# Optimization experiments

Hardware: AMD Instinct MI355X
Metric: run time of the kernel (lower is better)

## Reference

```python
import jax, jax.numpy as jnp
import numpy as np

V, C, L, D, H = 50257, 512, 6, 768, 12
HD = D // H
B, T = 4, 512
EPS = 1e-5


def setup_inputs() -> dict:
    key = jax.random.key(0)
    ks = jax.random.split(key, 24)
    s = 0.02
    inp = {
        'x': jax.random.randint(ks[0], (B, T), 0, V),
        'target': jax.random.randint(ks[1], (B, T), 0, V),
        'tok_emb': jax.random.normal(ks[2], (V, D), jnp.float32) * s,
        'pos_emb': jax.random.normal(ks[3], (C, D), jnp.float32) * s,
        'in_proj_w': jax.random.normal(ks[4], (L, D, D), jnp.float32) * s,
        'in_proj_b': jnp.zeros((L, D), jnp.float32),
        'wk': jax.random.normal(ks[5], (L, H, D, HD), jnp.float32) * s,
        'bk': jnp.zeros((L, H, HD), jnp.float32),
        'wq': jax.random.normal(ks[6], (L, H, D, HD), jnp.float32) * s,
        'bq': jnp.zeros((L, H, HD), jnp.float32),
        'wv': jax.random.normal(ks[7], (L, H, D, HD), jnp.float32) * s,
        'bv': jnp.zeros((L, H, HD), jnp.float32),
        'out_proj_w': jax.random.normal(ks[8], (L, D, D), jnp.float32) * s,
        'out_proj_b': jnp.zeros((L, D), jnp.float32),
        'ff_w1': jax.random.normal(ks[9], (L, D, 4 * D), jnp.float32) * s,
        'ff_b1': jnp.zeros((L, 4 * D), jnp.float32),
        'ff_w2': jax.random.normal(ks[10], (L, 4 * D, D), jnp.float32) * s,
        'ff_b2': jnp.zeros((L, D), jnp.float32),
        'lna_g': jnp.ones((L, D), jnp.float32),
        'lna_b': jnp.zeros((L, D), jnp.float32),
        'lnf_g': jnp.ones((L, D), jnp.float32),
        'lnf_b': jnp.zeros((L, D), jnp.float32),
        'out_w': jax.random.normal(ks[11], (D, V), jnp.float32) * s,
        'out_b': jnp.zeros((V,), jnp.float32),
    }
    return inp


def _ln(x, g, b):
    m = jnp.mean(x, axis=-1, keepdims=True)
    v = jnp.var(x, axis=-1, keepdims=True)
    return (x - m) * jax.lax.rsqrt(v + EPS) * g + b


def _gpt(x_ids, tok_emb, pos_emb, in_proj_w, in_proj_b, wk, bk, wq, bq, wv, bv,
         out_proj_w, out_proj_b, ff_w1, ff_b1, ff_w2, ff_b2,
         lna_g, lna_b, lnf_g, lnf_b, out_w, out_b):
    t = x_ids.shape[1]
    x = tok_emb[x_ids] + pos_emb[:t]  # [B,T,D]
    causal = jnp.tril(jnp.ones((t, t), bool))  # mask[t,s]
    for l in range(L):
        h = _ln(x, lna_g[l], lna_b[l])
        h = h @ in_proj_w[l] + in_proj_b[l]
        k = jnp.einsum('btd,hde->bhte', h, wk[l]) + bk[l][None, :, None, :]
        q = jnp.einsum('btd,hde->bhte', h, wq[l]) + bq[l][None, :, None, :]
        v = jnp.einsum('btd,hde->bhte', h, wv[l]) + bv[l][None, :, None, :]
        # Faithful quirk: scores = k @ q^T, NO 1/sqrt(d) scaling
        wei = jnp.einsum('bhte,bhse->bhts', k, q)
        wei = jnp.where(causal, wei, -jnp.inf)
        wei = jax.nn.softmax(wei, axis=-1)
        attn = jnp.einsum('bhts,bhse->bhte', wei, v)  # [B,H,T,HD]
        attn = attn.transpose(0, 2, 1, 3).reshape(x.shape[0], t, D)
        x = attn @ out_proj_w[l] + out_proj_b[l] + x
        h = _ln(x, lnf_g[l], lnf_b[l])
        h = jax.nn.relu(h @ ff_w1[l] + ff_b1[l]) @ ff_w2[l] + ff_b2[l]
        x = h + x
    logits = x @ out_w + out_b  # [B,T,V]
    return logits


def reference(x, target, tok_emb, pos_emb, in_proj_w, in_proj_b, wk, bk, wq, bq,
              wv, bv, out_proj_w, out_proj_b, ff_w1, ff_b1, ff_w2, ff_b2,
              lna_g, lna_b, lnf_g, lnf_b, out_w, out_b):
    logits = _gpt(x, tok_emb, pos_emb, in_proj_w, in_proj_b, wk, bk, wq, bq,
                  wv, bv, out_proj_w, out_proj_b, ff_w1, ff_b1, ff_w2, ff_b2,
                  lna_g, lna_b, lnf_g, lnf_b, out_w, out_b)
    logp = jax.nn.log_softmax(logits.reshape(-1, V), axis=-1)
    nll = -jnp.take_along_axis(logp, target.reshape(-1, 1), axis=-1)
    loss = jnp.mean(nll)
    return logits, loss
```

## Files before the change

### kernel.cpp

```cpp
#include <hip/hip_runtime.h>
#include <cstdint>
#include <cstddef>

static constexpr int kD   = 768;
static constexpr int kHD  = 64;
static constexpr int kNH  = 12;
static constexpr int kT   = 512;
static constexpr int kB   = 4;
static constexpr int kRows = kB * kT;
static constexpr int kV   = 50257;
static constexpr int kL   = 6;
static constexpr int kFF  = 3072;
static constexpr float kEps = 1e-5f;

typedef short bf16x8 __attribute__((ext_vector_type(8)));
typedef float f32x4  __attribute__((ext_vector_type(4)));
typedef unsigned short u16;
typedef unsigned short u16x4 __attribute__((ext_vector_type(4)));
typedef unsigned short u16x8 __attribute__((ext_vector_type(8)));

__device__ __forceinline__ void split1(float a, u16& h, u16& l)
{
    unsigned u = __float_as_uint(a);
    h = (u16)(u >> 16);
    float fh = __uint_as_float(u & 0xFFFF0000u);
    float r = a - fh;
    unsigned v = __float_as_uint(r);
    l = (u16)((v + 0x7FFFu + ((v >> 16) & 1u)) >> 16);
}

__global__ __launch_bounds__(256) void embed_kernel(
    const int* __restrict__ ids, const float* __restrict__ tok,
    const float* __restrict__ pos, float* __restrict__ x)
{
    int i = blockIdx.x * 256 + threadIdx.x;
    if (i >= kRows * kD) return;
    int row = i / kD, d = i - row * kD;
    x[i] = tok[(size_t)ids[row] * kD + d] + pos[(row % kT) * kD + d];
}

__global__ __launch_bounds__(256) void ln_kernel(
    const float* __restrict__ x, const float* __restrict__ g,
    const float* __restrict__ b, float* __restrict__ o)
{
    const int row = blockIdx.x;
    const float* xr = x + (size_t)row * kD;
    float s = 0.f, ss = 0.f;
    for (int d = threadIdx.x; d < kD; d += 256) {
        float v = xr[d];
        s += v; ss += v * v;
    }
    #pragma unroll
    for (int off = 32; off; off >>= 1) {
        s  += __shfl_xor(s, off);
        ss += __shfl_xor(ss, off);
    }
    __shared__ float sh_s[4], sh_ss[4];
    const int wid = threadIdx.x >> 6, lane = threadIdx.x & 63;
    if (lane == 0) { sh_s[wid] = s; sh_ss[wid] = ss; }
    __syncthreads();
    s  = sh_s[0] + sh_s[1] + sh_s[2] + sh_s[3];
    ss = sh_ss[0] + sh_ss[1] + sh_ss[2] + sh_ss[3];
    const float mean = s * (1.0f / kD);
    const float var  = ss * (1.0f / kD) - mean * mean;
    const float rstd = rsqrtf(var + kEps);
    float* orow = o + (size_t)row * kD;
    for (int d = threadIdx.x; d < kD; d += 256)
        orow[d] = (xr[d] - mean) * rstd * g[d] + b[d];
}

__global__ __launch_bounds__(256) void split_kernel(
    const float* __restrict__ in, u16* __restrict__ hi, u16* __restrict__ lo)
{
    const int i = blockIdx.x * 256 + threadIdx.x;
    float4 v = ((const float4*)in)[i];
    u16x4 hv, lv;
    u16 a, c;
    split1(v.x, a, c); hv[0] = a; lv[0] = c;
    split1(v.y, a, c); hv[1] = a; lv[1] = c;
    split1(v.z, a, c); hv[2] = a; lv[2] = c;
    split1(v.w, a, c); hv[3] = a; lv[3] = c;
    ((u16x4*)hi)[i] = hv;
    ((u16x4*)lo)[i] = lv;
}

__global__ __launch_bounds__(256) void repack_qkv_kernel(
    const float* __restrict__ wk, const float* __restrict__ wq,
    const float* __restrict__ wv, const float* __restrict__ bk,
    const float* __restrict__ bq, const float* __restrict__ bv,
    float* __restrict__ Wp, float* __restrict__ Bp)
{
    int i = blockIdx.x * 256 + threadIdx.x;
    if (i < 3 * kD) {
        int which = i / kD, c = i - which * kD;
        const float* bsrc = (which == 0) ? bk : (which == 1) ? bq : bv;
        Bp[i] = bsrc[c];
    }
    if (i >= kD * 3 * kD) return;
    int col = i % (3 * kD), d = i / (3 * kD);
    int which = col / kD, hc = col - which * kD;
    const float* src = (which == 0) ? wk : (which == 1) ? wq : wv;
    Wp[i] = src[(size_t)(hc >> 6) * (kD * kHD) + (size_t)d * kHD + (hc & 63)];
}

template<int BM>
__global__ __launch_bounds__(256) void gemm3_kernel(
    const u16* __restrict__ Ahi, const u16* __restrict__ Alo,
    const float* __restrict__ W, const float* __restrict__ bias,
    const float* __restrict__ resid, float* __restrict__ out,
    int N, int K, int relu)
{
    constexpr int LDT = 40;
    __shared__ u16 Ah[BM][LDT], Al[BM][LDT];
    __shared__ u16 Bh[128][LDT], Bl[128][LDT];
    const int tid = threadIdx.x;
    const int m0 = blockIdx.y * BM;
    const int n0 = blockIdx.x * 128;
    const int wid = tid >> 6, lane = tid & 63;
    const int wr = wid >> 1, wc = wid & 1;
    const int fr = lane & 15, fg = lane >> 4;
    constexpr int MF = BM / 32;

    f32x4 acc[MF][4];
    #pragma unroll
    for (int i = 0; i < MF; ++i)
        #pragma unroll
        for (int j = 0; j < 4; ++j) acc[i][j] = (f32x4){0.f, 0.f, 0.f, 0.f};

    const int bc  = tid >> 1;
    const int bk0 = (tid & 1) << 4;
    const bool bvalid = (n0 + bc) < N;

    for (int k0 = 0; k0 < K; k0 += 32) {
        for (int i = tid; i < BM * 4; i += 256) {
            const int r = i >> 2, q = (i & 3) << 3;
            const size_t off = (size_t)(m0 + r) * K + k0 + q;
            *(u16x8*)&Ah[r][q] = *(const u16x8*)(Ahi + off);
            *(u16x8*)&Al[r][q] = *(const u16x8*)(Alo + off);
        }
        {
            const float* wp = W + (size_t)(k0 + bk0) * N + (n0 + bc);
            float v[16];
            #pragma unroll
            for (int j = 0; j < 16; ++j)
                v[j] = bvalid ? wp[(size_t)j * N] : 0.f;
            #pragma unroll
            for (int j4 = 0; j4 < 4; ++j4) {
                u16x4 hh, ll;
                #pragma unroll
                for (int j = 0; j < 4; ++j) {
                    u16 h1, l1; split1(v[(j4 << 2) + j], h1, l1);
                    hh[j] = h1; ll[j] = l1;
                }
                *(u16x4*)&Bh[bc][bk0 + (j4 << 2)] = hh;
                *(u16x4*)&Bl[bc][bk0 + (j4 << 2)] = ll;
            }
        }
        __syncthreads();

        bf16x8 ah[MF], al[MF], bh[4], bl[4];
        #pragma unroll
        for (int f = 0; f < MF; ++f) {
            const int row = wr * (BM / 2) + (f << 4) + fr;
            ah[f] = *(const bf16x8*)&Ah[row][fg << 3];
            al[f] = *(const bf16x8*)&Al[row][fg << 3];
        }
        #pragma unroll
        for (int f = 0; f < 4; ++f) {
            const int col = (wc << 6) + (f << 4) + fr;
            bh[f] = *(const bf16x8*)&Bh[col][fg << 3];
            bl[f] = *(const bf16x8*)&Bl[col][fg << 3];
        }
        #pragma unroll
        for (int i = 0; i < MF; ++i)
            #pragma unroll
            for (int j = 0; j < 4; ++j) {
                acc[i][j] = __builtin_amdgcn_mfma_f32_16x16x32_bf16(ah[i], bh[j], acc[i][j], 0, 0, 0);
                acc[i][j] = __builtin_amdgcn_mfma_f32_16x16x32_bf16(ah[i], bl[j], acc[i][j], 0, 0, 0);
                acc[i][j] = __builtin_amdgcn_mfma_f32_16x16x32_bf16(al[i], bh[j], acc[i][j], 0, 0, 0);
            }
        __syncthreads();
    }

    #pragma unroll
    for (int i = 0; i < MF; ++i) {
        const int mb = m0 + wr * (BM / 2) + (i << 4) + (fg << 2);
        #pragma unroll
        for (int j = 0; j < 4; ++j) {
            const int n = n0 + (wc << 6) + (j << 4) + fr;
            if (n < N) {
                const float bvv = bias ? bias[n] : 0.f;
                #pragma unroll
                for (int r = 0; r < 4; ++r) {
                    const size_t oo = (size_t)(mb + r) * N + n;
                    float vv = acc[i][j][r] + bvv;
                    if (resid) vv += resid[oo];
                    if (relu)  vv = fmaxf(vv, 0.f);
                    out[oo] = vv;
                }
            }
        }
    }
}

__global__ __launch_bounds__(256) void attn2_kernel(
    const float* __restrict__ qkv, float* __restrict__ out)
{
    __shared__ float KbT[64][64];
    __shared__ float QbT[64][64];
    __shared__ float Vb[64][64];
    __shared__ float Pt[64][64];
    const int tb = gridDim.x - 1 - blockIdx.x;
    const int hh = blockIdx.y, b = blockIdx.z;
    const int t0 = tb << 6;
    const int tid = threadIdx.x;
    const int ty = tid >> 4, tx = tid & 15;
    const int sr = tid >> 2;
    const int se0 = (tid & 3) << 4;
    const size_t rb = (size_t)b * kT;

    {
        const float* ks = qkv + (rb + t0 + sr) * (3 * kD) + hh * kHD + se0;
        #pragma unroll
        for (int j = 0; j < 16; j += 4) {
            float4 v = *(const float4*)(ks + j);
            KbT[se0 + j + 0][sr] = v.x;
            KbT[se0 + j + 1][sr] = v.y;
            KbT[se0 + j + 2][sr] = v.z;
            KbT[se0 + j + 3][sr] = v.w;
        }
    }

    float m[4], l[4], O[4][4];
    #pragma unroll
    for (int i = 0; i < 4; ++i) {
        m[i] = -INFINITY; l[i] = 0.f;
        #pragma unroll
        for (int j = 0; j < 4; ++j) O[i][j] = 0.f;
    }

    for (int s0 = 0; s0 <= t0; s0 += 64) {
        __syncthreads();
        {
            const float* qs = qkv + (rb + s0 + sr) * (3 * kD) + kD + hh * kHD + se0;
            #pragma unroll
            for (int j = 0; j < 16; j += 4) {
                float4 v = *(const float4*)(qs + j);
                QbT[se0 + j + 0][sr] = v.x;
                QbT[se0 + j + 1][sr] = v.y;
                QbT[se0 + j + 2][sr] = v.z;
                QbT[se0 + j + 3][sr] = v.w;
            }
            const float* vs = qkv + (rb + s0 + sr) * (3 * kD) + 2 * kD + hh * kHD + se0;
            #pragma unroll
            for (int jq = 0; jq < 4; ++jq) {
                const int c4 = (se0 >> 2) + jq;
                *(float4*)&Vb[sr][(c4 ^ (sr & 15)) << 2] = *(const float4*)(vs + (jq << 2));
            }
        }
        __syncthreads();

        float S[4][4];
        #pragma unroll
        for (int i = 0; i < 4; ++i)
            #pragma unroll
            for (int j = 0; j < 4; ++j) S[i][j] = 0.f;

        #pragma unroll 8
        for (int e = 0; e < 64; ++e) {
            float4 ka = *(const float4*)&KbT[e][ty << 2];
            float4 qa = *(const float4*)&QbT[e][tx << 2];
            float a[4] = {ka.x, ka.y, ka.z, ka.w};
            float q[4] = {qa.x, qa.y, qa.z, qa.w};
            #pragma unroll
            for (int i = 0; i < 4; ++i)
                #pragma unroll
                for (int j = 0; j < 4; ++j)
                    S[i][j] = fmaf(a[i], q[j], S[i][j]);
        }

        if (s0 == t0) {
            #pragma unroll
            for (int i = 0; i < 4; ++i)
                #pragma unroll
                for (int j = 0; j < 4; ++j)
                    if (((tx << 2) + j) > ((ty << 2) + i)) S[i][j] = -INFINITY;
        }

        float p[4][4];
        #pragma unroll
        for (int i = 0; i < 4; ++i) {
            float mx = fmaxf(fmaxf(S[i][0], S[i][1]), fmaxf(S[i][2], S[i][3]));
            #pragma unroll
            for (int off = 1; off < 16; off <<= 1)
                mx = fmaxf(mx, __shfl_xor(mx, off));
            const float nm = fmaxf(m[i], mx);
            const float sc = __expf(m[i] - nm);
            float rs = 0.f;
            #pragma unroll
            for (int j = 0; j < 4; ++j) { p[i][j] = __expf(S[i][j] - nm); rs += p[i][j]; }
            #pragma unroll
            for (int off = 1; off < 16; off <<= 1) rs += __shfl_xor(rs, off);
            l[i] = l[i] * sc + rs;
            m[i] = nm;
            #pragma unroll
            for (int j = 0; j < 4; ++j) O[i][j] *= sc;
        }
        #pragma unroll
        for (int j = 0; j < 4; ++j) {
            const int scol = (tx << 2) + j;
            float4 pv = make_float4(p[0][j], p[1][j], p[2][j], p[3][j]);
            *(float4*)&Pt[scol][(ty ^ (scol & 15)) << 2] = pv;
        }
        __syncthreads();

        #pragma unroll 8
        for (int s = 0; s < 64; ++s) {
            float4 pa = *(const float4*)&Pt[s][(ty ^ (s & 15)) << 2];
            float4 va = *(const float4*)&Vb[s][(tx ^ (s & 15)) << 2];
            float a[4] = {pa.x, pa.y, pa.z, pa.w};
            float v[4] = {va.x, va.y, va.z, va.w};
            #pragma unroll
            for (int i = 0; i < 4; ++i)
                #pragma unroll
                for (int j = 0; j < 4; ++j)
                    O[i][j] = fmaf(a[i], v[j], O[i][j]);
        }
    }

    #pragma unroll
    for (int i = 0; i < 4; ++i) {
        const float inv = 1.0f / l[i];
        float4 o4 = make_float4(O[i][0] * inv, O[i][1] * inv, O[i][2] * inv, O[i][3] * inv);
        *(float4*)&out[(rb + t0 + (ty << 2) + i) * kD + hh * kHD + (tx << 2)] = o4;
    }
}

__global__ __launch_bounds__(256) void loss_kernel(
    const float* __restrict__ logits, const int* __restrict__ target,
    float* __restrict__ loss)
{
    const int row = blockIdx.x;
    const float* lr = logits + (size_t)row * kV;
    const int wid = threadIdx.x >> 6, lane = threadIdx.x & 63;
    __shared__ float red[4];

    float lmax = -INFINITY;
    for (int i = threadIdx.x; i < kV; i += 256) lmax = fmaxf(lmax, lr[i]);
    #pragma unroll
    for (int off = 32; off; off >>= 1) lmax = fmaxf(lmax, __shfl_xor(lmax, off));
    if (lane == 0) red[wid] = lmax;
    __syncthreads();
    lmax = fmaxf(fmaxf(red[0], red[1]), fmaxf(red[2], red[3]));
    __syncthreads();

    float lsum = 0.f;
    for (int i = threadIdx.x; i < kV; i += 256) lsum += __expf(lr[i] - lmax);
    #pragma unroll
    for (int off = 32; off; off >>= 1) lsum += __shfl_xor(lsum, off);
    if (lane == 0) red[wid] = lsum;
    __syncthreads();
    lsum = red[0] + red[1] + red[2] + red[3];

    if (threadIdx.x == 0) {
        float logZ = lmax + logf(lsum);
        float nll = logZ - lr[target[row]];
        atomicAdd(loss, nll * (1.0f / kRows));
    }
}

extern "C" void kernel_launch(void* const* d_in, const int* in_sizes, int n_in,
                              void* d_out, int out_size, void* d_ws, size_t ws_size,
                              hipStream_t stream)
{
    const int*   ids = (const int*)d_in[0];
    const int*   tgt = (const int*)d_in[1];
    const float* tok = (const float*)d_in[2];
    const float* pos = (const float*)d_in[3];
    const float* ipw = (const float*)d_in[4];
    const float* ipb = (const float*)d_in[5];
    const float* wk  = (const float*)d_in[6];
    const float* bk  = (const float*)d_in[7];
    const float* wq  = (const float*)d_in[8];
    const float* bq  = (const float*)d_in[9];
    const float* wv  = (const float*)d_in[10];
    const float* bv  = (const float*)d_in[11];
    const float* opw = (const float*)d_in[12];
    const float* opb = (const float*)d_in[13];
    const float* fw1 = (const float*)d_in[14];
    const float* fb1 = (const float*)d_in[15];
    const float* fw2 = (const float*)d_in[16];
    const float* fb2 = (const float*)d_in[17];
    const float* lag = (const float*)d_in[18];
    const float* lab = (const float*)d_in[19];
    const float* lfg = (const float*)d_in[20];
    const float* lfb = (const float*)d_in[21];
    const float* outw = (const float*)d_in[22];
    const float* outb = (const float*)d_in[23];

    float* ws = (float*)d_ws;
    const size_t S = (size_t)kRows * kD;
    float* x    = ws;
    float* h    = x    + S;
    float* h2   = h    + S;
    float* atb  = h2   + S;
    float* qkv  = atb  + S;
    float* ffh  = qkv  + 3 * S;
    float* wqkv = ffh  + 4 * S;
    float* bqkv = wqkv + (size_t)kD * 3 * kD;

    u16* sfA_hi = (u16*)ffh;  u16* sfA_lo = sfA_hi + S;
    u16* sqA_hi = (u16*)qkv;  u16* sqA_lo = sqA_hi + S;
    u16* sbA_hi = (u16*)h2;   u16* sbA_lo = sbA_hi + 4 * S;
    u16* shA_hi = (u16*)h;    u16* shA_lo = shA_hi + S;

    float* logits = (float*)d_out;
    float* loss = logits + (size_t)kRows * kV;

    embed_kernel<<<(kRows * kD + 255) / 256, 256, 0, stream>>>(ids, tok, pos, x);

    const size_t wsz = (size_t)kD * kD;
    const size_t fsz = (size_t)kD * kFF;
    const int splitS = (int)(S / 1024);
    for (int l = 0; l < kL; ++l) {
        ln_kernel<<<kRows, 256, 0, stream>>>(x, lag + l * kD, lab + l * kD, h);
        split_kernel<<<splitS, 256, 0, stream>>>(h, sfA_hi, sfA_lo);
        gemm3_kernel<64><<<dim3(6, 32), 256, 0, stream>>>(
            sfA_hi, sfA_lo, ipw + l * wsz, ipb + l * kD, nullptr, h2, kD, kD, 0);
        repack_qkv_kernel<<<(kD * 3 * kD + 255) / 256, 256, 0, stream>>>(
            wk + l * wsz, wq + l * wsz, wv + l * wsz,
            bk + l * kD, bq + l * kD, bv + l * kD, wqkv, bqkv);
        split_kernel<<<splitS, 256, 0, stream>>>(h2, sfA_hi, sfA_lo);
        gemm3_kernel<128><<<dim3(18, 16), 256, 0, stream>>>(
            sfA_hi, sfA_lo, wqkv, bqkv, nullptr, qkv, 3 * kD, kD, 0);
        attn2_kernel<<<dim3(kT / 64, kNH, kB), 256, 0, stream>>>(qkv, atb);
        split_kernel<<<splitS, 256, 0, stream>>>(atb, sfA_hi, sfA_lo);
        gemm3_kernel<64><<<dim3(6, 32), 256, 0, stream>>>(
            sfA_hi, sfA_lo, opw + l * wsz, opb + l * kD, x, x, kD, kD, 0);
        ln_kernel<<<kRows, 256, 0, stream>>>(x, lfg + l * kD, lfb + l * kD, h);
        split_kernel<<<splitS, 256, 0, stream>>>(h, sqA_hi, sqA_lo);
        gemm3_kernel<128><<<dim3(24, 16), 256, 0, stream>>>(
            sqA_hi, sqA_lo, fw1 + l * fsz, fb1 + l * kFF, nullptr, ffh, kFF, kD, 1);
        split_kernel<<<4 * splitS, 256, 0, stream>>>(ffh, sbA_hi, sbA_lo);
        gemm3_kernel<64><<<dim3(6, 32), 256, 0, stream>>>(
            sbA_hi, sbA_lo, fw2 + l * fsz, fb2 + l * kD, x, x, kD, kFF, 0);
    }
    split_kernel<<<splitS, 256, 0, stream>>>(x, shA_hi, shA_lo);
    gemm3_kernel<128><<<dim3((kV + 127) / 128, 16), 256, 0, stream>>>(
        shA_hi, shA_lo, outw, outb, nullptr, logits, kV, kD, 0);
    hipMemsetAsync(loss, 0, sizeof(float), stream);
    loss_kernel<<<kRows, 256, 0, stream>>>(logits, tgt, loss);
}
```

Before: 4.727 ms.

## Fuse bf16 split into producers, fp16 single-pass LM head, online-softmax loss

Removes the standalone split kernels by having layernorm, attention and GEMM epilogues write hi/lo bf16 pairs directly, saving fp32 round trips. The LDS tile layout in gemm3 changes to a k-group-major layout, and weight loads become 8-element coalesced column reads. The final vocabulary projection uses a new single-pass fp16 MFMA kernel instead of the three-pass split-bf16 GEMM, which lowers precision of the logits. The loss kernel becomes a one-pass online softmax.

New measurement: 5.143 ms. 1.09x slower.

```diff
diff --git a/kernel.cpp b/kernel.cpp
--- a/kernel.cpp
+++ b/kernel.cpp
@@ -18,6 +18,7 @@
 typedef unsigned short u16;
 typedef unsigned short u16x4 __attribute__((ext_vector_type(4)));
 typedef unsigned short u16x8 __attribute__((ext_vector_type(8)));
+typedef _Float16 f16x8 __attribute__((ext_vector_type(8)));
 
 __device__ __forceinline__ void split1(float a, u16& h, u16& l)
 {
@@ -29,6 +30,12 @@
     l = (u16)((v + 0x7FFFu + ((v >> 16) & 1u)) >> 16);
 }
 
+__device__ __forceinline__ u16 f16bits(float v)
+{
+    _Float16 t = (_Float16)v;
+    return __builtin_bit_cast(u16, t);
+}
+
 __global__ __launch_bounds__(256) void embed_kernel(
     const int* __restrict__ ids, const float* __restrict__ tok,
     const float* __restrict__ pos, float* __restrict__ x)
@@ -39,9 +46,9 @@
     x[i] = tok[(size_t)ids[row] * kD + d] + pos[(row % kT) * kD + d];
 }
 
-__global__ __launch_bounds__(256) void ln_kernel(
+__global__ __launch_bounds__(256) void ln_split_kernel(
     const float* __restrict__ x, const float* __restrict__ g,
-    const float* __restrict__ b, float* __restrict__ o)
+    const float* __restrict__ b, u16* __restrict__ ohi, u16* __restrict__ olo)
 {
     const int row = blockIdx.x;
     const float* xr = x + (size_t)row * kD;
@@ -64,24 +71,23 @@
     const float mean = s * (1.0f / kD);
     const float var  = ss * (1.0f / kD) - mean * mean;
     const float rstd = rsqrtf(var + kEps);
-    float* orow = o + (size_t)row * kD;
-    for (int d = threadIdx.x; d < kD; d += 256)
-        orow[d] = (xr[d] - mean) * rstd * g[d] + b[d];
-}
-
-__global__ __launch_bounds__(256) void split_kernel(
-    const float* __restrict__ in, u16* __restrict__ hi, u16* __restrict__ lo)
+    const size_t base = (size_t)row * kD;
+    for (int d = threadIdx.x; d < kD; d += 256) {
+        float val = (xr[d] - mean) * rstd * g[d] + b[d];
+        u16 h1, l1; split1(val, h1, l1);
+        ohi[base + d] = h1; olo[base + d] = l1;
+    }
+}
+
+__global__ __launch_bounds__(256) void cvt16_kernel(
+    const float* __restrict__ in, u16* __restrict__ out)
 {
     const int i = blockIdx.x * 256 + threadIdx.x;
     float4 v = ((const float4*)in)[i];
-    u16x4 hv, lv;
-    u16 a, c;
-    split1(v.x, a, c); hv[0] = a; lv[0] = c;
-    split1(v.y, a, c); hv[1] = a; lv[1] = c;
-    split1(v.z, a, c); hv[2] = a; lv[2] = c;
-    split1(v.w, a, c); hv[3] = a; lv[3] = c;
-    ((u16x4*)hi)[i] = hv;
-    ((u16x4*)lo)[i] = lv;
+    u16x4 o;
+    o[0] = f16bits(v.x); o[1] = f16bits(v.y);
+    o[2] = f16bits(v.z); o[3] = f16bits(v.w);
+    ((u16x4*)out)[i] = o;
 }
 
 __global__ __launch_bounds__(256) void repack_qkv_kernel(
@@ -108,11 +114,11 @@
     const u16* __restrict__ Ahi, const u16* __restrict__ Alo,
     const float* __restrict__ W, const float* __restrict__ bias,
     const float* __restrict__ resid, float* __restrict__ out,
+    u16* __restrict__ ohi, u16* __restrict__ olo,
     int N, int K, int relu)
 {
-    constexpr int LDT = 40;
-    __shared__ u16 Ah[BM][LDT], Al[BM][LDT];
-    __shared__ u16 Bh[128][LDT], Bl[128][LDT];
+    __shared__ u16 Ah[4][BM][8], Al[4][BM][8];
+    __shared__ u16 Bh[4][128][8], Bl[4][128][8];
     const int tid = threadIdx.x;
     const int m0 = blockIdx.y * BM;
     const int n0 = blockIdx.x * 128;
@@ -127,34 +133,29 @@
         #pragma unroll
         for (int j = 0; j < 4; ++j) acc[i][j] = (f32x4){0.f, 0.f, 0.f, 0.f};
 
-    const int bc  = tid >> 1;
-    const int bk0 = (tid & 1) << 4;
-    const bool bvalid = (n0 + bc) < N;
+    const int bc = tid & 127;
+    const int bg2 = tid >> 7;
+    const bool cval = (n0 + bc) < N;
 
     for (int k0 = 0; k0 < K; k0 += 32) {
         for (int i = tid; i < BM * 4; i += 256) {
-            const int r = i >> 2, q = (i & 3) << 3;
-            const size_t off = (size_t)(m0 + r) * K + k0 + q;
-            *(u16x8*)&Ah[r][q] = *(const u16x8*)(Ahi + off);
-            *(u16x8*)&Al[r][q] = *(const u16x8*)(Alo + off);
-        }
-        {
-            const float* wp = W + (size_t)(k0 + bk0) * N + (n0 + bc);
-            float v[16];
-            #pragma unroll
-            for (int j = 0; j < 16; ++j)
-                v[j] = bvalid ? wp[(size_t)j * N] : 0.f;
-            #pragma unroll
-            for (int j4 = 0; j4 < 4; ++j4) {
-                u16x4 hh, ll;
-                #pragma unroll
-                for (int j = 0; j < 4; ++j) {
-                    u16 h1, l1; split1(v[(j4 << 2) + j], h1, l1);
-                    hh[j] = h1; ll[j] = l1;
-                }
-                *(u16x4*)&Bh[bc][bk0 + (j4 << 2)] = hh;
-                *(u16x4*)&Bl[bc][bk0 + (j4 << 2)] = ll;
-            }
+            const int r = i >> 2, q = i & 3;
+            const size_t off = (size_t)(m0 + r) * K + k0 + (q << 3);
+            *(u16x8*)&Ah[q][r][0] = *(const u16x8*)(Ahi + off);
+            *(u16x8*)&Al[q][r][0] = *(const u16x8*)(Alo + off);
+        }
+        #pragma unroll
+        for (int f8 = 0; f8 < 2; ++f8) {
+            const int q = (bg2 << 1) + f8;
+            u16x8 hh, ll;
+            #pragma unroll
+            for (int j = 0; j < 8; ++j) {
+                float v = cval ? W[(size_t)(k0 + (q << 3) + j) * N + (n0 + bc)] : 0.f;
+                u16 h1, l1; split1(v, h1, l1);
+                hh[j] = h1; ll[j] = l1;
+            }
+            *(u16x8*)&Bh[q][bc][0] = hh;
+            *(u16x8*)&Bl[q][bc][0] = ll;
         }
         __syncthreads();
 
@@ -162,14 +163,14 @@
         #pragma unroll
         for (int f = 0; f < MF; ++f) {
             const int row = wr * (BM / 2) + (f << 4) + fr;
-            ah[f] = *(const bf16x8*)&Ah[row][fg << 3];
-            al[f] = *(const bf16x8*)&Al[row][fg << 3];
+            ah[f] = *(const bf16x8*)&Ah[fg][row][0];
+            al[f] = *(const bf16x8*)&Al[fg][row][0];
         }
         #pragma unroll
         for (int f = 0; f < 4; ++f) {
             const int col = (wc << 6) + (f << 4) + fr;
-            bh[f] = *(const bf16x8*)&Bh[col][fg << 3];
-            bl[f] = *(const bf16x8*)&Bl[col][fg << 3];
+            bh[f] = *(const bf16x8*)&Bh[fg][col][0];
+            bl[f] = *(const bf16x8*)&Bl[fg][col][0];
         }
         #pragma unroll
         for (int i = 0; i < MF; ++i)
@@ -196,15 +197,86 @@
                     float vv = acc[i][j][r] + bvv;
                     if (resid) vv += resid[oo];
                     if (relu)  vv = fmaxf(vv, 0.f);
-                    out[oo] = vv;
+                    if (ohi) { u16 h1, l1; split1(vv, h1, l1); ohi[oo] = h1; olo[oo] = l1; }
+                    else     out[oo] = vv;
                 }
             }
         }
     }
 }
 
+__global__ __launch_bounds__(512) void gemmh_kernel(
+    const u16* __restrict__ Axh, const float* __restrict__ W,
+    const float* __restrict__ bias, float* __restrict__ out, int N, int K)
+{
+    __shared__ _Float16 Ah[4][256][8];
+    __shared__ _Float16 Bh[4][128][8];
+    const int tid = threadIdx.x;
+    const int m0 = blockIdx.x * 256;
+    const int n0 = blockIdx.y * 128;
+    const int wid = tid >> 6, lane = tid & 63;
+    const int wr = wid >> 1, wc = wid & 1;
+    const int fr = lane & 15, fg = lane >> 4;
+
+    f32x4 acc[4][4];
+    #pragma unroll
+    for (int i = 0; i < 4; ++i)
+        #pragma unroll
+        for (int j = 0; j < 4; ++j) acc[i][j] = (f32x4){0.f, 0.f, 0.f, 0.f};
+
+    const int bc = tid & 127, bg = tid >> 7;
+    const bool cval = (n0 + bc) < N;
+
+    for (int k0 = 0; k0 < K; k0 += 32) {
+        for (int i = tid; i < 1024; i += 512) {
+            const int r = i >> 2, q = i & 3;
+            *(u16x8*)&Ah[q][r][0] =
+                *(const u16x8*)(Axh + (size_t)(m0 + r) * K + k0 + (q << 3));
+        }
+        {
+            f16x8 hv;
+            #pragma unroll
+            for (int j = 0; j < 8; ++j) {
+                float v = cval ? W[(size_t)(k0 + (bg << 3) + j) * N + (n0 + bc)] : 0.f;
+                hv[j] = (_Float16)v;
+            }
+            *(f16x8*)&Bh[bg][bc][0] = hv;
+        }
+        __syncthreads();
+
+        f16x8 a[4], bb[4];
+        #pragma unroll
+        for (int f = 0; f < 4; ++f)
+            a[f] = *(const f16x8*)&Ah[fg][(wr << 6) + (f << 4) + fr][0];
+        #pragma unroll
+        for (int j = 0; j < 4; ++j)
+            bb[j] = *(const f16x8*)&Bh[fg][(wc << 6) + (j << 4) + fr][0];
+        #pragma unroll
+        for (int f = 0; f < 4; ++f)
+            #pragma unroll
+            for (int j = 0; j < 4; ++j)
+                acc[f][j] = __builtin_amdgcn_mfma_f32_16x16x32_f16(a[f], bb[j], acc[f][j], 0, 0, 0);
+        __syncthreads();
+    }
+
+    #pragma unroll
+    for (int f = 0; f < 4; ++f) {
+        const int mb = m0 + (wr << 6) + (f << 4) + (fg << 2);
+        #pragma unroll
+        for (int j = 0; j < 4; ++j) {
+            const int n = n0 + (wc << 6) + (j << 4) + fr;
+            if (n < N) {
+                const float bvv = bias[n];
+                #pragma unroll
+                for (int r = 0; r < 4; ++r)
+                    out[(size_t)(mb + r) * N + n] = acc[f][j][r] + bvv;
+            }
+        }
+    }
+}
+
 __global__ __launch_bounds__(256) void attn2_kernel(
-    const float* __restrict__ qkv, float* __restrict__ out)
+    const float* __restrict__ qkv, u16* __restrict__ ohi, u16* __restrict__ olo)
 {
     __shared__ float KbT[64][64];
     __shared__ float QbT[64][64];
@@ -331,8 +403,15 @@
     #pragma unroll
     for (int i = 0; i < 4; ++i) {
         const float inv = 1.0f / l[i];
-        float4 o4 = make_float4(O[i][0] * inv, O[i][1] * inv, O[i][2] * inv, O[i][3] * inv);
-        *(float4*)&out[(rb + t0 + (ty << 2) + i) * kD + hh * kHD + (tx << 2)] = o4;
+        const size_t oo = (rb + t0 + (ty << 2) + i) * kD + hh * kHD + (tx << 2);
+        u16x4 oh, ol;
+        #pragma unroll
+        for (int j = 0; j < 4; ++j) {
+            u16 h1, l1; split1(O[i][j] * inv, h1, l1);
+            oh[j] = h1; ol[j] = l1;
+        }
+        *(u16x4*)&ohi[oo] = oh;
+        *(u16x4*)&olo[oo] = ol;
     }
 }
 
@@ -343,30 +422,57 @@
     const int row = blockIdx.x;
     const float* lr = logits + (size_t)row * kV;
     const int wid = threadIdx.x >> 6, lane = threadIdx.x & 63;
-    __shared__ float red[4];
-
-    float lmax = -INFINITY;
-    for (int i = threadIdx.x; i < kV; i += 256) lmax = fmaxf(lmax, lr[i]);
-    #pragma unroll
-    for (int off = 32; off; off >>= 1) lmax = fmaxf(lmax, __shfl_xor(lmax, off));
-    if (lane == 0) red[wid] = lmax;
+    __shared__ float redm[4], reds[4];
+
+    float m = -INFINITY, s = 0.f;
+    for (int i = threadIdx.x; i < kV; i += 256) {
+        float v = lr[i];
+        if (v <= m) {
+            s += __expf(v - m);
+        } else {
+            s = s * __expf(m - v) + 1.f;
+            m = v;
+        }
+    }
+    #pragma unroll
+    for (int off = 32; off; off >>= 1) {
+        float mo = __shfl_xor(m, off), so = __shfl_xor(s, off);
+        float nm = fmaxf(m, mo);
+        s = s * __expf(m - nm) + so * __expf(mo - nm);
+        m = nm;
+    }
+    if (lane == 0) { redm[wid] = m; reds[wid] = s; }
     __syncthreads();
-    lmax = fmaxf(fmaxf(red[0], red[1]), fmaxf(red[2], red[3]));
-    __syncthreads();
-
-    float lsum = 0.f;
-    for (int i = threadIdx.x; i < kV; i += 256) lsum += __expf(lr[i] - lmax);
-    #pragma unroll
-    for (int off = 32; off; off >>= 1) lsum += __shfl_xor(lsum, off);
-    if (lane == 0) red[wid] = lsum;
-    __syncthreads();
-    lsum = red[0] + red[1] + red[2] + red[3];
 
     if (threadIdx.x == 0) {
-        float logZ = lmax + logf(lsum);
+        m = redm[0]; s = reds[0];
+        #pragma unroll
+        for (int w = 1; w < 4; ++w) {
+            float nm = fmaxf(m, redm[w]);
+            s = s * __expf(m - nm) + reds[w] * __expf(redm[w] - nm);
+            m = nm;
+        }
+        float logZ = m + logf(s);
         float nll = logZ - lr[target[row]];
         atomicAdd(loss, nll * (1.0f / kRows));
     }
+}
+
+static inline void launch_gemm3_64(const u16* Ahi, const u16* Alo, const float* W,
+                                   const float* bias, const float* resid,
+                                   float* out, u16* ohi, u16* olo,
+                                   int N, int K, int relu, hipStream_t stream)
+{
+    gemm3_kernel<64><<<dim3((N + 127) / 128, kRows / 64), 256, 0, stream>>>(
+        Ahi, Alo, W, bias, resid, out, ohi, olo, N, K, relu);
+}
+static inline void launch_gemm3_128(const u16* Ahi, const u16* Alo, const float* W,
+                                    const float* bias, const float* resid,
+                                    float* out, u16* ohi, u16* olo,
+                                    int N, int K, int relu, hipStream_t stream)
+{
+    gemm3_kernel<128><<<dim3((N + 127) / 128, kRows / 128), 256, 0, stream>>>(
+        Ahi, Alo, W, bias, resid, out, ohi, olo, N, K, relu);
 }
 
 extern "C" void kernel_launch(void* const* d_in, const int* in_sizes, int n_in,
@@ -400,19 +506,20 @@
 
     float* ws = (float*)d_ws;
     const size_t S = (size_t)kRows * kD;
-    float* x    = ws;
-    float* h    = x    + S;
-    float* h2   = h    + S;
-    float* atb  = h2   + S;
-    float* qkv  = atb  + S;
-    float* ffh  = qkv  + 3 * S;
-    float* wqkv = ffh  + 4 * S;
-    float* bqkv = wqkv + (size_t)kD * 3 * kD;
-
-    u16* sfA_hi = (u16*)ffh;  u16* sfA_lo = sfA_hi + S;
-    u16* sqA_hi = (u16*)qkv;  u16* sqA_lo = sqA_hi + S;
-    u16* sbA_hi = (u16*)h2;   u16* sbA_lo = sbA_hi + 4 * S;
-    u16* shA_hi = (u16*)h;    u16* shA_lo = shA_hi + S;
+    float* x      = ws;
+    float* hbuf   = x    + S;
+    float* h2buf  = hbuf + S;
+    float* atbbuf = h2buf + S;
+    float* qkv    = atbbuf + S;
+    float* ffhbuf = qkv  + 3 * S;
+    float* wqkv   = ffhbuf + 4 * S;
+    float* bqkv   = wqkv + (size_t)kD * 3 * kD;
+
+    u16* h_hi  = (u16*)hbuf;   u16* h_lo  = h_hi  + S;
+    u16* h2_hi = (u16*)h2buf;  u16* h2_lo = h2_hi + S;
+    u16* at_hi = (u16*)atbbuf; u16* at_lo = at_hi + S;
+    u16* ff_hi = (u16*)ffhbuf; u16* ff_lo = ff_hi + 4 * S;
+    u16* xh    = (u16*)hbuf;
 
     float* logits = (float*)d_out;
     float* loss = logits + (size_t)kRows * kV;
@@ -421,33 +528,29 @@
 
     const size_t wsz = (size_t)kD * kD;
     const size_t fsz = (size_t)kD * kFF;
-    const int splitS = (int)(S / 1024);
     for (int l = 0; l < kL; ++l) {
-        ln_kernel<<<kRows, 256, 0, stream>>>(x, lag + l * kD, lab + l * kD, h);
-        split_kernel<<<splitS, 256, 0, stream>>>(h, sfA_hi, sfA_lo);
-        gemm3_kernel<64><<<dim3(6, 32), 256, 0, stream>>>(
-            sfA_hi, sfA_lo, ipw + l * wsz, ipb + l * kD, nullptr, h2, kD, kD, 0);
+        ln_split_kernel<<<kRows, 256, 0, stream>>>(x, lag + l * kD, lab + l * kD,
+                                                   h_hi, h_lo);
+        launch_gemm3_64(h_hi, h_lo, ipw + l * wsz, ipb + l * kD, nullptr,
+                        nullptr, h2_hi, h2_lo, kD, kD, 0, stream);
         repack_qkv_kernel<<<(kD * 3 * kD + 255) / 256, 256, 0, stream>>>(
             wk + l * wsz, wq + l * wsz, wv + l * wsz,
             bk + l * kD, bq + l * kD, bv + l * kD, wqkv, bqkv);
-        split_kernel<<<splitS, 256, 0, stream>>>(h2, sfA_hi, sfA_lo);
-        gemm3_kernel<128><<<dim3(18, 16), 256, 0, stream>>>(
-            sfA_hi, sfA_lo, wqkv, bqkv, nullptr, qkv, 3 * kD, kD, 0);
-        attn2_kernel<<<dim3(kT / 64, kNH, kB), 256, 0, stream>>>(qkv, atb);
-        split_kernel<<<splitS, 256, 0, stream>>>(atb, sfA_hi, sfA_lo);
-        gemm3_kernel<64><<<dim3(6, 32), 256, 0, stream>>>(
-            sfA_hi, sfA_lo, opw + l * wsz, opb + l * kD, x, x, kD, kD, 0);
-        ln_kernel<<<kRows, 256, 0, stream>>>(x, lfg + l * kD, lfb + l * kD, h);
-        split_kernel<<<splitS, 256, 0, stream>>>(h, sqA_hi, sqA_lo);
-        gemm3_kernel<128><<<dim3(24, 16), 256, 0, stream>>>(
-            sqA_hi, sqA_lo, fw1 + l * fsz, fb1 + l * kFF, nullptr, ffh, kFF, kD, 1);
-        split_kernel<<<4 * splitS, 256, 0, stream>>>(ffh, sbA_hi, sbA_lo);
-        gemm3_kernel<64><<<dim3(6, 32), 256, 0, stream>>>(
-            sbA_hi, sbA_lo, fw2 + l * fsz, fb2 + l * kD, x, x, kD, kFF, 0);
-    }
-    split_kernel<<<splitS, 256, 0, stream>>>(x, shA_hi, shA_lo);
-    gemm3_kernel<128><<<dim3((kV + 127) / 128, 16), 256, 0, stream>>>(
-        shA_hi, shA_lo, outw, outb, nullptr, logits, kV, kD, 0);
+        launch_gemm3_128(h2_hi, h2_lo, wqkv, bqkv, nullptr,
+                         qkv, nullptr, nullptr, 3 * kD, kD, 0, stream);
+        attn2_kernel<<<dim3(kT / 64, kNH, kB), 256, 0, stream>>>(qkv, at_hi, at_lo);
+        launch_gemm3_64(at_hi, at_lo, opw + l * wsz, opb + l * kD, x,
+                        x, nullptr, nullptr, kD, kD, 0, stream);
+        ln_split_kernel<<<kRows, 256, 0, stream>>>(x, lfg + l * kD, lfb + l * kD,
+                                                   h_hi, h_lo);
+        launch_gemm3_128(h_hi, h_lo, fw1 + l * fsz, fb1 + l * kFF, nullptr,
+                         nullptr, ff_hi, ff_lo, kFF, kD, 1, stream);
+        launch_gemm3_64(ff_hi, ff_lo, fw2 + l * fsz, fb2 + l * kD, x,
+                        x, nullptr, nullptr, kD, kFF, 0, stream);
+    }
+    cvt16_kernel<<<(int)(S / 1024), 256, 0, stream>>>(x, xh);
+    gemmh_kernel<<<dim3(kRows / 256, (kV + 127) / 128), 512, 0, stream>>>(
+        xh, outw, outb, logits, kV, kD);
     hipMemsetAsync(loss, 0, sizeof(float), stream);
     loss_kernel<<<kRows, 256, 0, stream>>>(logits, tgt, loss);
 }
```
